# Performance work log

Measured on AMD Instinct MI355X. Metric: run time of the kernel, lower is better.

Reference implementation:

```python
import math
import itertools
import jax, jax.numpy as jnp
import numpy as np

QUALITY = 95
FACTOR = (200.0 - 2.0 * QUALITY) / 100.0  # quality>=50 branch -> 0.1

# ---- constant tables (match original torch Parameters) ----
_Y = np.array([
    [16, 11, 10, 16, 24, 40, 51, 61],
    [12, 12, 14, 19, 26, 58, 60, 55],
    [14, 13, 16, 24, 40, 57, 69, 56],
    [14, 17, 22, 29, 51, 87, 80, 62],
    [18, 22, 37, 56, 68, 109, 103, 77],
    [24, 35, 55, 64, 81, 104, 113, 92],
    [49, 64, 78, 87, 103, 121, 120, 101],
    [72, 92, 95, 98, 112, 100, 103, 99]], dtype=np.float32)
Y_TABLE = jnp.asarray(_Y.T)
_C = np.full((8, 8), 99.0, dtype=np.float32)
_C[:4, :4] = np.array([[17, 18, 24, 47], [18, 21, 26, 66],
                       [24, 26, 56, 99], [47, 66, 99, 99]], dtype=np.float32).T
C_TABLE = jnp.asarray(_C)

RGB2YCBCR = jnp.asarray(np.array([
    [0.299, 0.587, 0.114],
    [-0.168736, -0.331264, 0.5],
    [0.5, -0.418688, -0.081312]], dtype=np.float32))
YCBCR2RGB = jnp.asarray(np.array([
    [1.0, 0.0, 1.402],
    [1.0, -0.344136, -0.714136],
    [1.0, 1.772, 0.0]], dtype=np.float32))

_cosmat = np.cos((2 * np.arange(8)[:, None] + 1) * np.arange(8)[None, :] * np.pi / 16).astype(np.float32)  # [x,u]
DCT_T = jnp.asarray(np.einsum('xu,yv->xyuv', _cosmat, _cosmat))   # tensor[x,y,u,v]
IDCT_T = jnp.asarray(np.einsum('ux,vy->xyuv', _cosmat, _cosmat))  # cos((2u+1)x..)cos((2v+1)y..)
_alpha = np.array([1.0 / np.sqrt(2)] + [1.0] * 7, dtype=np.float32)
ALPHA = jnp.asarray(np.outer(_alpha, _alpha))
DCT_SCALE = ALPHA * 0.25


def diff_round(x):
    s = jnp.zeros_like(x)
    for n in range(1, 10):
        s = s + ((-1.0) ** (n + 1) / n) * jnp.sin(2.0 * math.pi * n * x)
    return x - s / math.pi


def _avgpool2(x):  # [B,H,W] -> [B,H/2,W/2]
    b, h, w = x.shape
    return x.reshape(b, h // 2, 2, w // 2, 2).mean(axis=(2, 4))


def _block_split(x):  # [B,H,W] -> [B,N,8,8]
    b, h, w = x.shape
    return x.reshape(b, h // 8, 8, w // 8, 8).transpose(0, 1, 3, 2, 4).reshape(b, -1, 8, 8)


def _block_merge(p, h, w):  # [B,N,8,8] -> [B,h,w]
    b = p.shape[0]
    return p.reshape(b, h // 8, w // 8, 8, 8).transpose(0, 1, 3, 2, 4).reshape(b, h, w)


def _compress_component(comp, table):
    blocks = _block_split(comp) - 128.0
    dct = DCT_SCALE * jnp.einsum('bnxy,xyuv->bnuv', blocks, DCT_T)
    return diff_round(dct / (table * FACTOR))


def _decompress_component(q, table, h, w):
    d = q * (table * FACTOR)
    idct = 0.25 * jnp.einsum('bnxy,xyuv->bnuv', d * ALPHA, IDCT_T) + 128.0
    return _block_merge(idct, h, w)


def _diffjpeg(x):
    b, c, h, w = x.shape
    img = x * 255.0
    # RGB -> YCbCr (pixel @ RGB2YCBCR.T) + shift
    ycbcr = jnp.einsum('bchw,oc->bhwo', img, RGB2YCBCR) + jnp.array([0.0, 128.0, 128.0], dtype=x.dtype)
    y = ycbcr[..., 0]
    cb = _avgpool2(ycbcr[..., 1])
    cr = _avgpool2(ycbcr[..., 2])
    # compress
    yq = _compress_component(y, Y_TABLE)
    cbq = _compress_component(cb, C_TABLE)
    crq = _compress_component(cr, C_TABLE)
    # decompress
    y2 = _decompress_component(yq, Y_TABLE, h, w)
    cb2 = _decompress_component(cbq, C_TABLE, h // 2, w // 2)
    cr2 = _decompress_component(crq, C_TABLE, h // 2, w // 2)
    cb_up = jnp.repeat(jnp.repeat(cb2, 2, axis=1), 2, axis=2)
    cr_up = jnp.repeat(jnp.repeat(cr2, 2, axis=1), 2, axis=2)
    ycc = jnp.stack([y2, cb_up, cr_up], axis=3)  # [B,H,W,3]
    rgb = jnp.einsum('bhwc,oc->bhwo', ycc + jnp.array([0.0, -128.0, -128.0], dtype=x.dtype), YCBCR2RGB)
    rgb = rgb.transpose(0, 3, 1, 2)  # [B,3,H,W]
    rgb = jnp.clip(rgb, 0.0, 255.0)
    return rgb / 255.0


def setup_inputs() -> dict:
    key = jax.random.key(0)
    x = jax.random.uniform(key, (16, 3, 512, 512), dtype=jnp.float32)
    return {"x": x}


def reference(x):
    return _diffjpeg(x)
```

## Files before the change

### kernel.cpp

```cpp
#include <hip/hip_runtime.h>


__device__ constexpr float YTAB8[8][8] = {
    {16, 12, 14, 14, 18, 24, 49, 72},
    {11, 12, 13, 17, 22, 35, 64, 92},
    {10, 14, 16, 22, 37, 55, 78, 95},
    {16, 19, 24, 29, 56, 64, 87, 98},
    {24, 26, 40, 51, 68, 81, 103, 112},
    {40, 58, 57, 87, 109, 104, 121, 100},
    {51, 60, 69, 80, 103, 113, 120, 103},
    {61, 55, 56, 62, 77, 92, 101, 99}};

__device__ constexpr float CTAB8[8][8] = {
    {17, 18, 24, 47, 99, 99, 99, 99},
    {18, 21, 26, 66, 99, 99, 99, 99},
    {24, 26, 56, 99, 99, 99, 99, 99},
    {47, 66, 99, 99, 99, 99, 99, 99},
    {99, 99, 99, 99, 99, 99, 99, 99},
    {99, 99, 99, 99, 99, 99, 99, 99},
    {99, 99, 99, 99, 99, 99, 99, 99},
    {99, 99, 99, 99, 99, 99, 99, 99}};

#define C1f 0.9807852804032304f
#define C2f 0.9238795325112867f
#define C3f 0.8314696123025452f
#define C4f 0.7071067811865476f
#define C5f 0.5555702330196022f
#define C6f 0.3826834323650898f
#define C7f 0.1950903220161283f

__device__ __forceinline__ void dct8(float y[8]) {
    float e0=y[0]+y[7], e1=y[1]+y[6], e2=y[2]+y[5], e3=y[3]+y[4];
    float o0=y[0]-y[7], o1=y[1]-y[6], o2=y[2]-y[5], o3=y[3]-y[4];
    float t0=e0+e3, t1=e1+e2, d0=e0-e3, d1=e1-e2;
    y[0]=t0+t1; y[4]=(t0-t1)*C4f;
    y[2]=d0*C2f+d1*C6f; y[6]=d0*C6f-d1*C2f;
    y[1]=o0*C1f+o1*C3f+o2*C5f+o3*C7f;
    y[3]=o0*C3f-o1*C7f-o2*C1f-o3*C5f;
    y[5]=o0*C5f-o1*C1f+o2*C7f+o3*C3f;
    y[7]=o0*C7f-o1*C5f+o2*C3f-o3*C1f;
}

__device__ __forceinline__ void idct8(float y[8]) {
    float a=y[4]*C4f, p=y[0]+a, m=y[0]-a;
    float q=y[2]*C2f+y[6]*C6f, w=y[2]*C6f-y[6]*C2f;
    float E0=p+q, E1=m+w, E2=m-w, E3=p-q;
    float O0=y[1]*C1f+y[3]*C3f+y[5]*C5f+y[7]*C7f;
    float O1=y[1]*C3f-y[3]*C7f-y[5]*C1f-y[7]*C5f;
    float O2=y[1]*C5f-y[3]*C1f+y[5]*C7f+y[7]*C3f;
    float O3=y[1]*C7f-y[3]*C5f+y[5]*C3f-y[7]*C1f;
    y[0]=E0+O0; y[7]=E0-O0; y[1]=E1+O1; y[6]=E1-O1;
    y[2]=E2+O2; y[5]=E2-O2; y[3]=E3+O3; y[4]=E3-O3;
}

__device__ __forceinline__ void transpose8(float y[8]) {
    const int lane = threadIdx.x & 63;
#pragma unroll
    for (int s = 1; s <= 4; s <<= 1) {
        const bool upper = (lane & (s << 3)) != 0;
#pragma unroll
        for (int j = 0; j < 8; ++j) {
            if ((j & s) == 0) {
                float a = y[j], b2 = y[j | s];
                float t = upper ? a : b2;
                t = __shfl_xor(t, s << 3, 64);
                if (upper) y[j] = t; else y[j | s] = t;
            }
        }
    }
}

__device__ __forceinline__ void wave_lds_fence() {
    __builtin_amdgcn_wave_barrier();
    asm volatile("s_waitcnt lgkmcnt(0)" ::: "memory");
    __builtin_amdgcn_wave_barrier();
}

__device__ __forceinline__ float diff_round_f(float x) {
    float f = __builtin_amdgcn_fractf(x);
    float sc = __builtin_amdgcn_sinf(f);
    float c1v = __builtin_amdgcn_cosf(f);
    float twoc = 2.0f * c1v;
    float sp = 0.0f, acc = 0.0f;
    const float coef[9] = {1.0f, -0.5f, 1.0f/3.0f, -0.25f, 0.2f,
                           -1.0f/6.0f, 1.0f/7.0f, -0.125f, 1.0f/9.0f};
#pragma unroll
    for (int n = 0; n < 9; ++n) {
        acc += coef[n] * sc;
        float sn = twoc * sc - sp;
        sp = sc; sc = sn;
    }
    return x - acc * 0.3183098861837907f;
}

__device__ __forceinline__ void jpeg_block(float y[8], const float* qs, int r) {
    dct8(y); transpose8(y); dct8(y);
#pragma unroll
    for (int j = 0; j < 8; ++j) {
        float s1v = qs[2 * (j * 8 + r)];
        float s2v = qs[2 * (j * 8 + r) + 1];
        y[j] = diff_round_f(y[j] * s1v) * s2v;
    }
    idct8(y); transpose8(y); idct8(y);
}

struct Raw { float4 R0, R1, G0, G1, B0, B1; };

#define PLANE ((size_t)512 * 512)

__device__ __forceinline__ Raw issue_load(const float* __restrict__ src,
                                          int py, int px) {
    const float* p = src + (size_t)py * 512 + px;
    Raw L;
    L.R0 = *(const float4*)(p);
    L.R1 = *(const float4*)(p + 4);
    L.G0 = *(const float4*)(p + PLANE);
    L.G1 = *(const float4*)(p + PLANE + 4);
    L.B0 = *(const float4*)(p + 2 * PLANE);
    L.B1 = *(const float4*)(p + 2 * PLANE + 4);
    return L;
}

__device__ __forceinline__ void convert_pool(const Raw& L, float y[8],
                                             float cb[4], float cr[4]) {
    y[0] = 76.245f*L.R0.x + 149.685f*L.G0.x + 29.07f*L.B0.x - 128.0f;
    y[1] = 76.245f*L.R0.y + 149.685f*L.G0.y + 29.07f*L.B0.y - 128.0f;
    y[2] = 76.245f*L.R0.z + 149.685f*L.G0.z + 29.07f*L.B0.z - 128.0f;
    y[3] = 76.245f*L.R0.w + 149.685f*L.G0.w + 29.07f*L.B0.w - 128.0f;
    y[4] = 76.245f*L.R1.x + 149.685f*L.G1.x + 29.07f*L.B1.x - 128.0f;
    y[5] = 76.245f*L.R1.y + 149.685f*L.G1.y + 29.07f*L.B1.y - 128.0f;
    y[6] = 76.245f*L.R1.z + 149.685f*L.G1.z + 29.07f*L.B1.z - 128.0f;
    y[7] = 76.245f*L.R1.w + 149.685f*L.G1.w + 29.07f*L.B1.w - 128.0f;
    float rh0=L.R0.x+L.R0.y, rh1=L.R0.z+L.R0.w, rh2=L.R1.x+L.R1.y, rh3=L.R1.z+L.R1.w;
    float gh0=L.G0.x+L.G0.y, gh1=L.G0.z+L.G0.w, gh2=L.G1.x+L.G1.y, gh3=L.G1.z+L.G1.w;
    float bh0=L.B0.x+L.B0.y, bh1=L.B0.z+L.B0.w, bh2=L.B1.x+L.B1.y, bh3=L.B1.z+L.B1.w;
    const float kbr = -10.75692f, kbg = -21.11808f, kbb = 31.875f;
    const float krr =  31.875f,   krg = -26.69136f, krb = -5.18364f;
    cb[0]=kbr*rh0+kbg*gh0+kbb*bh0; cb[1]=kbr*rh1+kbg*gh1+kbb*bh1;
    cb[2]=kbr*rh2+kbg*gh2+kbb*bh2; cb[3]=kbr*rh3+kbg*gh3+kbb*bh3;
    cr[0]=krr*rh0+krg*gh0+krb*bh0; cr[1]=krr*rh1+krg*gh1+krb*bh1;
    cr[2]=krr*rh2+krg*gh2+krb*bh2; cr[3]=krr*rh3+krg*gh3+krb*bh3;
#pragma unroll
    for (int k = 0; k < 4; ++k) {
        cb[k] += __shfl_xor(cb[k], 8, 64);
        cr[k] += __shfl_xor(cr[k], 8, 64);
    }
}

__device__ __forceinline__ void process_store(
        float y[8], const float cb[4], const float cr[4],
        float* __restrict__ dst, int py, int px,
        const float (*QS)[128], float (*PL)[8][17], float (*CL)[8][17],
        int r, int b, int br, int bc) {
    if (!(r & 1)) {
        const int prow = br * 4 + (r >> 1);
        const int pc = bc * 4;
#pragma unroll
        for (int k = 0; k < 4; ++k) {
            PL[0][prow][pc + k] = cb[k];
            PL[1][prow][pc + k] = cr[k];
        }
    }
    wave_lds_fence();

    jpeg_block(y, QS[0], r);

    {
        const int ch = (b >> 1) & 1;
        const int cblk = b & 1;
        float c[8];
#pragma unroll
        for (int j = 0; j < 8; ++j) c[j] = PL[ch][r][cblk * 8 + j];
        jpeg_block(c, QS[1], r);
        if (b < 4) {
#pragma unroll
            for (int j = 0; j < 8; ++j) CL[ch][r][cblk * 8 + j] = c[j];
        }
    }
    wave_lds_fence();

    const int prow = br * 4 + (r >> 1);
    const int pc = bc * 4;
    float cbv[4], crv[4];
#pragma unroll
    for (int jj = 0; jj < 4; ++jj) {
        cbv[jj] = CL[0][prow][pc + jj];
        crv[jj] = CL[1][prow][pc + jj];
    }
    float* p = dst + (size_t)py * 512 + px;
    float o[8];
#pragma unroll
    for (int j = 0; j < 8; ++j) {
        float v = (y[j] + 128.0f) + 1.402f * crv[j >> 1];
        o[j] = fminf(fmaxf(v, 0.0f), 255.0f) * (1.0f / 255.0f);
    }
    *(float4*)(p)     = make_float4(o[0], o[1], o[2], o[3]);
    *(float4*)(p + 4) = make_float4(o[4], o[5], o[6], o[7]);
#pragma unroll
    for (int j = 0; j < 8; ++j) {
        float v = (y[j] + 128.0f) - 0.344136f * cbv[j >> 1] - 0.714136f * crv[j >> 1];
        o[j] = fminf(fmaxf(v, 0.0f), 255.0f) * (1.0f / 255.0f);
    }
    *(float4*)(p + PLANE)     = make_float4(o[0], o[1], o[2], o[3]);
    *(float4*)(p + PLANE + 4) = make_float4(o[4], o[5], o[6], o[7]);
#pragma unroll
    for (int j = 0; j < 8; ++j) {
        float v = (y[j] + 128.0f) + 1.772f * cbv[j >> 1];
        o[j] = fminf(fmaxf(v, 0.0f), 255.0f) * (1.0f / 255.0f);
    }
    *(float4*)(p + 2 * PLANE)     = make_float4(o[0], o[1], o[2], o[3]);
    *(float4*)(p + 2 * PLANE + 4) = make_float4(o[4], o[5], o[6], o[7]);
}

__global__ __launch_bounds__(128, 4) void diffjpeg_kernel(
        const float* __restrict__ x, float* __restrict__ out) {
    __shared__ float QS[2][128];
    __shared__ float PLs[2][2][8][17];
    __shared__ float CLs[2][2][8][17];

    const int tid = threadIdx.x;
    {
        int type = tid >> 6;
        int k = tid & 63, u = k >> 3, v = k & 7;
        float t = (type ? CTAB8[u][v] : YTAB8[u][v]) * 0.1f;
        float aa = 0.25f * ((u == 0) ? C4f : 1.0f) * ((v == 0) ? C4f : 1.0f);
        QS[type][2 * k]     = aa / t;
        QS[type][2 * k + 1] = aa * t;
    }
    __syncthreads();

    const int wv = tid >> 6;
    const int lane = tid & 63;
    const int r = lane >> 3;
    const int b = lane & 7;
    const int br = b >> 2, bc = b & 3;

    const int wave_gid = blockIdx.x * 2 + wv;

    const int sid0 = wave_gid;
    const int img0 = sid0 >> 9, loc0 = sid0 & 511;
    const int py0 = (loc0 >> 4) * 16 + br * 8 + r;
    const int px0 = (loc0 & 15) * 32 + bc * 8;
    const float* src0 = x + (size_t)img0 * 3 * PLANE;

    const int sid1 = wave_gid + 4096;
    const int img1 = sid1 >> 9, loc1 = sid1 & 511;
    const int py1 = (loc1 >> 4) * 16 + br * 8 + r;
    const int px1 = (loc1 & 15) * 32 + bc * 8;
    const float* src1 = x + (size_t)img1 * 3 * PLANE;

    Raw L0 = issue_load(src0, py0, px0);

    float y0[8], cb0[4], cr0[4];
    convert_pool(L0, y0, cb0, cr0);

    Raw L1 = issue_load(src1, py1, px1);

    process_store(y0, cb0, cr0, out + (size_t)img0 * 3 * PLANE, py0, px0,
                  QS, PLs[wv], CLs[wv], r, b, br, bc);

    float y1[8], cb1[4], cr1[4];
    convert_pool(L1, y1, cb1, cr1);

    process_store(y1, cb1, cr1, out + (size_t)img1 * 3 * PLANE, py1, px1,
                  QS, PLs[wv], CLs[wv], r, b, br, bc);
}

extern "C" void kernel_launch(void* const* d_in, const int* in_sizes, int n_in,
                              void* d_out, int out_size, void* d_ws, size_t ws_size,
                              hipStream_t stream) {
    const float* x = (const float*)d_in[0];
    float* out = (float*)d_out;
    dim3 grid(2048);
    dim3 block(128);
    diffjpeg_kernel<<<grid, block, 0, stream>>>(x, out);
}
```

Measured before the change: 25.74 us.

## Remap wave to 16x64 strip so chroma blocks need no redundant DCTs

Each wave now handles a 16x64 pixel strip: every lane processes two vertically stacked luma blocks, and the 8 lanes per row together cover 4 Cb plus 4 Cr chroma blocks. Before, each wave processed two separate 16x32 strips and recomputed a chroma jpeg_block on every lane, keeping only half of the results. The new mapping cuts the chroma DCT passes and needs one fewer LDS fence round. It also widens the LDS layout to 36-float rows so chroma planes can be read and written with float4 and float2 accesses. The trade-off is that both loads are issued at the start, which may raise register pressure and change the global access pattern.

Result: faster. 24.33 us (-5.5%).

```diff
diff --git a/kernel.cpp b/kernel.cpp
--- a/kernel.cpp
+++ b/kernel.cpp
@@ -97,9 +97,8 @@
     dct8(y); transpose8(y); dct8(y);
 #pragma unroll
     for (int j = 0; j < 8; ++j) {
-        float s1v = qs[2 * (j * 8 + r)];
-        float s2v = qs[2 * (j * 8 + r) + 1];
-        y[j] = diff_round_f(y[j] * s1v) * s2v;
+        float2 sv = *(const float2*)&qs[2 * (j * 8 + r)];
+        y[j] = diff_round_f(y[j] * sv.x) * sv.y;
     }
     idct8(y); transpose8(y); idct8(y);
 }
@@ -147,46 +146,13 @@
     }
 }
 
-__device__ __forceinline__ void process_store(
-        float y[8], const float cb[4], const float cr[4],
-        float* __restrict__ dst, int py, int px,
-        const float (*QS)[128], float (*PL)[8][17], float (*CL)[8][17],
-        int r, int b, int br, int bc) {
-    if (!(r & 1)) {
-        const int prow = br * 4 + (r >> 1);
-        const int pc = bc * 4;
-#pragma unroll
-        for (int k = 0; k < 4; ++k) {
-            PL[0][prow][pc + k] = cb[k];
-            PL[1][prow][pc + k] = cr[k];
-        }
-    }
-    wave_lds_fence();
-
-    jpeg_block(y, QS[0], r);
-
-    {
-        const int ch = (b >> 1) & 1;
-        const int cblk = b & 1;
-        float c[8];
-#pragma unroll
-        for (int j = 0; j < 8; ++j) c[j] = PL[ch][r][cblk * 8 + j];
-        jpeg_block(c, QS[1], r);
-        if (b < 4) {
-#pragma unroll
-            for (int j = 0; j < 8; ++j) CL[ch][r][cblk * 8 + j] = c[j];
-        }
-    }
-    wave_lds_fence();
-
-    const int prow = br * 4 + (r >> 1);
-    const int pc = bc * 4;
-    float cbv[4], crv[4];
-#pragma unroll
-    for (int jj = 0; jj < 4; ++jj) {
-        cbv[jj] = CL[0][prow][pc + jj];
-        crv[jj] = CL[1][prow][pc + jj];
-    }
+__device__ __forceinline__ void combine_store(
+        const float y[8], const float (*CL)[8][36],
+        float* __restrict__ dst, int py, int px, int prow, int b) {
+    float4 cb4 = *(const float4*)&CL[0][prow][b * 4];
+    float4 cr4 = *(const float4*)&CL[1][prow][b * 4];
+    const float cbv[4] = {cb4.x, cb4.y, cb4.z, cb4.w};
+    const float crv[4] = {cr4.x, cr4.y, cr4.z, cr4.w};
     float* p = dst + (size_t)py * 512 + px;
     float o[8];
 #pragma unroll
@@ -215,8 +181,8 @@
 __global__ __launch_bounds__(128, 4) void diffjpeg_kernel(
         const float* __restrict__ x, float* __restrict__ out) {
     __shared__ float QS[2][128];
-    __shared__ float PLs[2][2][8][17];
-    __shared__ float CLs[2][2][8][17];
+    __shared__ float PLs[2][2][8][36];
+    __shared__ float CLs[2][2][8][36];
 
     const int tid = threadIdx.x;
     {
@@ -233,37 +199,60 @@
     const int lane = tid & 63;
     const int r = lane >> 3;
     const int b = lane & 7;
-    const int br = b >> 2, bc = b & 3;
+
+    float (*PL)[8][36] = PLs[wv];
+    float (*CL)[8][36] = CLs[wv];
 
     const int wave_gid = blockIdx.x * 2 + wv;
-
-    const int sid0 = wave_gid;
-    const int img0 = sid0 >> 9, loc0 = sid0 & 511;
-    const int py0 = (loc0 >> 4) * 16 + br * 8 + r;
-    const int px0 = (loc0 & 15) * 32 + bc * 8;
-    const float* src0 = x + (size_t)img0 * 3 * PLANE;
-
-    const int sid1 = wave_gid + 4096;
-    const int img1 = sid1 >> 9, loc1 = sid1 & 511;
-    const int py1 = (loc1 >> 4) * 16 + br * 8 + r;
-    const int px1 = (loc1 & 15) * 32 + bc * 8;
-    const float* src1 = x + (size_t)img1 * 3 * PLANE;
-
-    Raw L0 = issue_load(src0, py0, px0);
-
-    float y0[8], cb0[4], cr0[4];
-    convert_pool(L0, y0, cb0, cr0);
-
-    Raw L1 = issue_load(src1, py1, px1);
-
-    process_store(y0, cb0, cr0, out + (size_t)img0 * 3 * PLANE, py0, px0,
-                  QS, PLs[wv], CLs[wv], r, b, br, bc);
-
-    float y1[8], cb1[4], cr1[4];
-    convert_pool(L1, y1, cb1, cr1);
-
-    process_store(y1, cb1, cr1, out + (size_t)img1 * 3 * PLANE, py1, px1,
-                  QS, PLs[wv], CLs[wv], r, b, br, bc);
+    const int img = wave_gid >> 8;
+    const int loc = wave_gid & 255;
+    const int sy = (loc >> 3) * 16;
+    const int sx = (loc & 7) * 64;
+    const float* src = x + (size_t)img * 3 * PLANE;
+    float* dst = out + (size_t)img * 3 * PLANE;
+
+    const int px  = sx + b * 8;
+    const int pyA = sy + r;
+    const int pyB = sy + 8 + r;
+
+    Raw LA = issue_load(src, pyA, px);
+    Raw LB = issue_load(src, pyB, px);
+
+    float yA[8], cbA[4], crA[4];
+    convert_pool(LA, yA, cbA, crA);
+    if (!(r & 1)) {
+        const int prow = r >> 1;
+        *(float4*)&PL[0][prow][b * 4] = make_float4(cbA[0], cbA[1], cbA[2], cbA[3]);
+        *(float4*)&PL[1][prow][b * 4] = make_float4(crA[0], crA[1], crA[2], crA[3]);
+    }
+    float yB[8], cbB[4], crB[4];
+    convert_pool(LB, yB, cbB, crB);
+    if (!(r & 1)) {
+        const int prow = 4 + (r >> 1);
+        *(float4*)&PL[0][prow][b * 4] = make_float4(cbB[0], cbB[1], cbB[2], cbB[3]);
+        *(float4*)&PL[1][prow][b * 4] = make_float4(crB[0], crB[1], crB[2], crB[3]);
+    }
+    wave_lds_fence();
+
+    jpeg_block(yA, QS[0], r);
+    jpeg_block(yB, QS[0], r);
+
+    {
+        const int ch = b >> 2;
+        const int cblk = b & 3;
+        float c[8];
+        float4 c0 = *(const float4*)&PL[ch][r][cblk * 8];
+        float4 c1 = *(const float4*)&PL[ch][r][cblk * 8 + 4];
+        c[0]=c0.x; c[1]=c0.y; c[2]=c0.z; c[3]=c0.w;
+        c[4]=c1.x; c[5]=c1.y; c[6]=c1.z; c[7]=c1.w;
+        jpeg_block(c, QS[1], r);
+        *(float4*)&CL[ch][r][cblk * 8]     = make_float4(c[0], c[1], c[2], c[3]);
+        *(float4*)&CL[ch][r][cblk * 8 + 4] = make_float4(c[4], c[5], c[6], c[7]);
+    }
+    wave_lds_fence();
+
+    combine_store(yA, CL, dst, pyA, px, (r >> 1), b);
+    combine_store(yB, CL, dst, pyB, px, 4 + (r >> 1), b);
 }
 
 extern "C" void kernel_launch(void* const* d_in, const int* in_sizes, int n_in,
```
